# Kernel optimization log

Hardware: AMD Instinct MI355X
Metric: run time of the kernel (lower is better)

Reference implementation:

```python
import jax, jax.numpy as jnp
import numpy as np

N_NODES = 50000
N_EDGES = 800000
D_IN = 512
D_OUT = 128

def setup_inputs() -> dict:
    key = jax.random.key(0)
    k1, k2, k3, k4, k5, k6 = jax.random.split(key, 6)
    std = 1.0 / np.sqrt(D_OUT)
    x = jax.random.normal(k1, (N_NODES, D_IN), dtype=jnp.float32)
    edge_w = jax.random.uniform(k2, (N_EDGES,), dtype=jnp.float32)
    src = jax.random.randint(k3, (N_EDGES,), 0, N_NODES, dtype=jnp.int32)
    dst = jax.random.randint(k4, (N_EDGES,), 0, N_NODES, dtype=jnp.int32)
    W = jax.random.uniform(k5, (D_IN, D_OUT), minval=-std, maxval=std, dtype=jnp.float32)
    b = jax.random.uniform(k6, (D_OUT,), minval=-std, maxval=std, dtype=jnp.float32)
    return {"x": x, "edge_w": edge_w, "src": src, "dst": dst, "W": W, "b": b}

def reference(x, edge_w, src, dst, W, b):
    # Dense GEMM: [N, D_in] @ [D_in, D_out]
    h = x @ W
    # SpMM with COO adjacency: out[i] = sum_{e: dst[e]==i} edge_w[e] * h[src[e]]
    msg = h[src] * edge_w[:, None]          # [E, D_out]
    agg = jax.ops.segment_sum(msg, dst, num_segments=N_NODES)
    return agg + b
```

## Files before the change

### kernel.cpp

```cpp
#include <hip/hip_runtime.h>
#include <hip/hip_bf16.h>

#define M_NODES  50000
#define D_IN_K   512
#define D_OUT_N  128
#define N_EDGES  800000
#define SCAN_NBLK 49
#define PAD 16

typedef short  bf16x8 __attribute__((ext_vector_type(8)));
typedef float  f32x4  __attribute__((ext_vector_type(4)));

static __device__ __forceinline__ unsigned short f2bf(float f) {
    unsigned u = __float_as_uint(f);
    unsigned r = u + 0x7FFF + ((u >> 16) & 1);
    return (unsigned short)(r >> 16);
}
static __device__ __forceinline__ float bflo(unsigned q) { return __uint_as_float(q << 16); }
static __device__ __forceinline__ float bfhi(unsigned q) { return __uint_as_float(q & 0xFFFF0000u); }

__global__ __launch_bounds__(256) void permw_kernel(const float* __restrict__ W,
                                                    unsigned short* __restrict__ Wp) {
    int tid = blockIdx.x * 256 + threadIdx.x;
    int lane = tid & 63;
    int nt   = (tid >> 6) & 7;
    int kb4  = tid >> 9;
    int n    = nt * 16 + (lane & 15);
    int kbase = kb4 * 32 + ((lane >> 4) & 3) * 8;
    unsigned short frag[8];
#pragma unroll
    for (int j = 0; j < 8; ++j)
        frag[j] = f2bf(W[(size_t)(kbase + j) * D_OUT_N + n]);
    *(uint4*)&Wp[(size_t)tid * 8] = *(const uint4*)frag;
}

__global__ __launch_bounds__(256, 2) void mfma_gemm_hist_kernel(const float* __restrict__ x,
                                                                const uint4* __restrict__ Wp4,
                                                                unsigned short* __restrict__ h,
                                                                const int* __restrict__ dst,
                                                                int* __restrict__ counts) {
    __shared__ uint4 wlds[4096];

    const int wave = threadIdx.x >> 6;
    const int lane = threadIdx.x & 63;
    const int m0   = blockIdx.x * 128 + wave * 32;
    const int mrow = lane & 15;
    const int kgrp = lane >> 4;

    const int r0 = m0 + mrow;
    const int r1 = m0 + 16 + mrow;
    const float* xr0 = x + (size_t)((r0 < M_NODES) ? r0 : M_NODES - 1) * D_IN_K + kgrp * 8;
    const float* xr1 = x + (size_t)((r1 < M_NODES) ? r1 : M_NODES - 1) * D_IN_K + kgrp * 8;

    f32x4 acc[2][8];
#pragma unroll
    for (int f = 0; f < 2; ++f)
#pragma unroll
        for (int t = 0; t < 8; ++t) acc[f][t] = (f32x4){0.f, 0.f, 0.f, 0.f};

    for (int half = 0; half < 2; ++half) {
        __syncthreads();
#pragma unroll
        for (int i = 0; i < 16; ++i)
            wlds[threadIdx.x + i * 256] = Wp4[half * 4096 + threadIdx.x + i * 256];
        __syncthreads();

        const float* px0 = xr0 + half * 256;
        const float* px1 = xr1 + half * 256;

        float4 a00 = *(const float4*)(px0);
        float4 a01 = *(const float4*)(px0 + 4);
        float4 a10 = *(const float4*)(px1);
        float4 a11 = *(const float4*)(px1 + 4);

#pragma unroll
        for (int kb = 0; kb < 8; ++kb) {
            float4 n00, n01, n10, n11;
            if (kb < 7) {
                n00 = *(const float4*)(px0 + (kb + 1) * 32);
                n01 = *(const float4*)(px0 + (kb + 1) * 32 + 4);
                n10 = *(const float4*)(px1 + (kb + 1) * 32);
                n11 = *(const float4*)(px1 + (kb + 1) * 32 + 4);
            }

            union { bf16x8 v; __hip_bfloat162 h2[4]; } c0, c1;
            c0.h2[0] = __float22bfloat162_rn(make_float2(a00.x, a00.y));
            c0.h2[1] = __float22bfloat162_rn(make_float2(a00.z, a00.w));
            c0.h2[2] = __float22bfloat162_rn(make_float2(a01.x, a01.y));
            c0.h2[3] = __float22bfloat162_rn(make_float2(a01.z, a01.w));
            c1.h2[0] = __float22bfloat162_rn(make_float2(a10.x, a10.y));
            c1.h2[1] = __float22bfloat162_rn(make_float2(a10.z, a10.w));
            c1.h2[2] = __float22bfloat162_rn(make_float2(a11.x, a11.y));
            c1.h2[3] = __float22bfloat162_rn(make_float2(a11.z, a11.w));
            bf16x8 a0 = c0.v, a1 = c1.v;

#pragma unroll
            for (int nt = 0; nt < 8; ++nt) {
                union { uint4 u; bf16x8 v; } wb;
                wb.u = wlds[(kb * 8 + nt) * 64 + lane];
                acc[0][nt] = __builtin_amdgcn_mfma_f32_16x16x32_bf16(a0, wb.v, acc[0][nt], 0, 0, 0);
                acc[1][nt] = __builtin_amdgcn_mfma_f32_16x16x32_bf16(a1, wb.v, acc[1][nt], 0, 0, 0);
            }

            if (kb < 7) { a00 = n00; a01 = n01; a10 = n10; a11 = n11; }
        }
    }

#pragma unroll
    for (int f = 0; f < 2; ++f)
#pragma unroll
        for (int r = 0; r < 4; ++r) {
            int rr = m0 + f * 16 + kgrp * 4 + r;
            if (rr < M_NODES) {
                unsigned short* hp = h + (size_t)rr * D_OUT_N + mrow;
#pragma unroll
                for (int nt = 0; nt < 8; ++nt)
                    hp[nt * 16] = f2bf(acc[f][nt][r]);
            }
        }

    const int epb = (N_EDGES + gridDim.x - 1) / gridDim.x;
    const int e0  = blockIdx.x * epb;
    const int e1  = (e0 + epb < N_EDGES) ? e0 + epb : N_EDGES;
    for (int e = e0 + threadIdx.x; e < e1; e += 256)
        atomicAdd(&counts[dst[e] * PAD], 1);
}

__global__ __launch_bounds__(256) void scan_kernel(const int* __restrict__ counts,
                                                   int* __restrict__ offsets,
                                                   int* __restrict__ cursor,
                                                   int* __restrict__ partials,
                                                   int* __restrict__ flags) {
    __shared__ int wsum[4];
    __shared__ int carry_s;
    const int tid  = threadIdx.x;
    const int lane = tid & 63;
    const int wid  = tid >> 6;
    const int blk  = blockIdx.x;
    const int base = blk * 1024 + tid * 4;

    int v[4];
#pragma unroll
    for (int i = 0; i < 4; ++i)
        v[i] = (base + i < M_NODES) ? counts[(base + i) * PAD] : 0;
    int t = v[0] + v[1] + v[2] + v[3];

    int s = t;
#pragma unroll
    for (int d = 1; d < 64; d <<= 1) {
        int u = __shfl_up(s, d, 64);
        if (lane >= d) s += u;
    }
    if (lane == 63) wsum[wid] = s;
    __syncthreads();
    int wbase = 0;
#pragma unroll
    for (int w = 0; w < 4; ++w) wbase += (w < wid) ? wsum[w] : 0;
    int total = wsum[0] + wsum[1] + wsum[2] + wsum[3];

    if (tid == 0) {
        __hip_atomic_store(&partials[blk], total, __ATOMIC_RELAXED, __HIP_MEMORY_SCOPE_AGENT);
        __hip_atomic_store(&flags[blk], 1, __ATOMIC_RELEASE, __HIP_MEMORY_SCOPE_AGENT);
        if (blk == 0) offsets[M_NODES] = N_EDGES;
    }

    if (wid == 0) {
        int val = 0;
        if (lane < blk) {
            while (__hip_atomic_load(&flags[lane], __ATOMIC_ACQUIRE, __HIP_MEMORY_SCOPE_AGENT) == 0) {}
            val = __hip_atomic_load(&partials[lane], __ATOMIC_RELAXED, __HIP_MEMORY_SCOPE_AGENT);
        }
#pragma unroll
        for (int d = 32; d > 0; d >>= 1) val += __shfl_xor(val, d, 64);
        if (lane == 0) carry_s = val;
    }
    __syncthreads();
    const int carry = carry_s;

    int run = carry + wbase + s - t;
#pragma unroll
    for (int i = 0; i < 4; ++i) {
        if (base + i < M_NODES) {
            offsets[base + i] = run;
            cursor[(base + i) * PAD] = run;
        }
        run += v[i];
    }
}

__global__ __launch_bounds__(256) void fill_kernel(const int* __restrict__ src,
                                                   const int* __restrict__ dst,
                                                   const float* __restrict__ edge_w,
                                                   int* __restrict__ cursor,
                                                   int2* __restrict__ ep) {
    int e = blockIdx.x * blockDim.x + threadIdx.x;
    if (e >= N_EDGES) return;
    int d   = dst[e];
    int pos = atomicAdd(&cursor[d * PAD], 1);
    ep[pos] = make_int2(src[e], __float_as_int(edge_w[e]));
}

__global__ __launch_bounds__(256) void gather_kernel(const unsigned short* __restrict__ h,
                                                     const int2* __restrict__ ep,
                                                     const int* __restrict__ offsets,
                                                     const float* __restrict__ b,
                                                     float* __restrict__ out) {
    int t    = blockIdx.x * blockDim.x + threadIdx.x;
    int node = t >> 4;
    int lane = t & 15;
    if (node >= M_NODES) return;
    int beg = offsets[node];
    int end = offsets[node + 1];

    float4 b0 = *(const float4*)&b[lane * 8];
    float4 b1 = *(const float4*)&b[lane * 8 + 4];
    float a[4][8];
#pragma unroll
    for (int u = 0; u < 4; ++u)
#pragma unroll
        for (int c = 0; c < 8; ++c) a[u][c] = 0.f;

    int j = beg;
    for (; j + 4 <= end; j += 4) {
        int2 e0 = ep[j], e1 = ep[j + 1], e2 = ep[j + 2], e3 = ep[j + 3];
        uint4 q0 = *(const uint4*)(h + (size_t)e0.x * D_OUT_N + lane * 8);
        uint4 q1 = *(const uint4*)(h + (size_t)e1.x * D_OUT_N + lane * 8);
        uint4 q2 = *(const uint4*)(h + (size_t)e2.x * D_OUT_N + lane * 8);
        uint4 q3 = *(const uint4*)(h + (size_t)e3.x * D_OUT_N + lane * 8);
        float w0 = __int_as_float(e0.y), w1 = __int_as_float(e1.y);
        float w2 = __int_as_float(e2.y), w3 = __int_as_float(e3.y);
        a[0][0] += w0 * bflo(q0.x);  a[0][1] += w0 * bfhi(q0.x);
        a[0][2] += w0 * bflo(q0.y);  a[0][3] += w0 * bfhi(q0.y);
        a[0][4] += w0 * bflo(q0.z);  a[0][5] += w0 * bfhi(q0.z);
        a[0][6] += w0 * bflo(q0.w);  a[0][7] += w0 * bfhi(q0.w);
        a[1][0] += w1 * bflo(q1.x);  a[1][1] += w1 * bfhi(q1.x);
        a[1][2] += w1 * bflo(q1.y);  a[1][3] += w1 * bfhi(q1.y);
        a[1][4] += w1 * bflo(q1.z);  a[1][5] += w1 * bfhi(q1.z);
        a[1][6] += w1 * bflo(q1.w);  a[1][7] += w1 * bfhi(q1.w);
        a[2][0] += w2 * bflo(q2.x);  a[2][1] += w2 * bfhi(q2.x);
        a[2][2] += w2 * bflo(q2.y);  a[2][3] += w2 * bfhi(q2.y);
        a[2][4] += w2 * bflo(q2.z);  a[2][5] += w2 * bfhi(q2.z);
        a[2][6] += w2 * bflo(q2.w);  a[2][7] += w2 * bfhi(q2.w);
        a[3][0] += w3 * bflo(q3.x);  a[3][1] += w3 * bfhi(q3.x);
        a[3][2] += w3 * bflo(q3.y);  a[3][3] += w3 * bfhi(q3.y);
        a[3][4] += w3 * bflo(q3.z);  a[3][5] += w3 * bfhi(q3.z);
        a[3][6] += w3 * bflo(q3.w);  a[3][7] += w3 * bfhi(q3.w);
    }
    for (; j < end; ++j) {
        int2 e0 = ep[j];
        float w0 = __int_as_float(e0.y);
        uint4 q0 = *(const uint4*)(h + (size_t)e0.x * D_OUT_N + lane * 8);
        a[0][0] += w0 * bflo(q0.x);  a[0][1] += w0 * bfhi(q0.x);
        a[0][2] += w0 * bflo(q0.y);  a[0][3] += w0 * bfhi(q0.y);
        a[0][4] += w0 * bflo(q0.z);  a[0][5] += w0 * bfhi(q0.z);
        a[0][6] += w0 * bflo(q0.w);  a[0][7] += w0 * bfhi(q0.w);
    }

    float4 o0 = make_float4(b0.x + a[0][0] + a[1][0] + a[2][0] + a[3][0],
                            b0.y + a[0][1] + a[1][1] + a[2][1] + a[3][1],
                            b0.z + a[0][2] + a[1][2] + a[2][2] + a[3][2],
                            b0.w + a[0][3] + a[1][3] + a[2][3] + a[3][3]);
    float4 o1 = make_float4(b1.x + a[0][4] + a[1][4] + a[2][4] + a[3][4],
                            b1.y + a[0][5] + a[1][5] + a[2][5] + a[3][5],
                            b1.z + a[0][6] + a[1][6] + a[2][6] + a[3][6],
                            b1.w + a[0][7] + a[1][7] + a[2][7] + a[3][7]);
    float* op = &out[(size_t)node * D_OUT_N + lane * 8];
    *(float4*)op = o0;
    *(float4*)(op + 4) = o1;
}

extern "C" void kernel_launch(void* const* d_in, const int* in_sizes, int n_in,
                              void* d_out, int out_size, void* d_ws, size_t ws_size,
                              hipStream_t stream) {
    const float* x      = (const float*)d_in[0];
    const float* edge_w = (const float*)d_in[1];
    const int*   src    = (const int*)d_in[2];
    const int*   dst    = (const int*)d_in[3];
    const float* W      = (const float*)d_in[4];
    const float* b      = (const float*)d_in[5];
    float* out = (float*)d_out;

    char* wsp = (char*)d_ws;
    unsigned short* h = (unsigned short*)wsp;  wsp += (size_t)M_NODES * D_OUT_N * 2;
    int*   counts   = (int*)wsp;         wsp += (size_t)M_NODES * PAD * 4;
    int*   flags    = (int*)wsp;         wsp += 64 * 4;
    int*   cursor   = (int*)wsp;         wsp += (size_t)M_NODES * PAD * 4;
    int*   offsets  = (int*)wsp;         wsp += (((size_t)M_NODES + 1) * 4 + 15) & ~15ull;
    int2*  ep       = (int2*)wsp;        wsp += (size_t)N_EDGES * 8;
    unsigned short* Wp = (unsigned short*)wsp; wsp += (size_t)16 * 8 * 64 * 8 * 2;
    int*   partials = (int*)wsp;         wsp += (SCAN_NBLK * 4 + 15) & ~15ull;

    hipMemsetAsync(counts, 0, (size_t)M_NODES * PAD * 4 + 64 * 4, stream);
    permw_kernel<<<32, 256, 0, stream>>>(W, Wp);
    mfma_gemm_hist_kernel<<<(M_NODES + 127) / 128, 256, 0, stream>>>(
        x, (const uint4*)Wp, h, dst, counts);
    scan_kernel<<<SCAN_NBLK, 256, 0, stream>>>(counts, offsets, cursor, partials, flags);
    fill_kernel<<<(N_EDGES + 255) / 256, 256, 0, stream>>>(src, dst, edge_w, cursor, ep);
    gather_kernel<<<(int)(((long long)M_NODES * 16 + 255) / 256), 256, 0, stream>>>(
        h, ep, offsets, b, out);
}
```

Measured before the change: 290.4 us.

## Double-buffer W via direct global-to-LDS loads, shrink GEMM tiles, unpad counters

The GEMM kernel now streams W through a 2x16KB double buffer with global_load_lds, prefetching the next K chunk while computing the current one. It also halves the per-block M tile to 64 rows and raises the occupancy hint to 4 blocks per CU, so LDS per block shrinks and more blocks are resident. Separately, the per-node count and cursor arrays drop the 16-int padding, which shrinks the memset and lets the scan use vector loads, at the cost of more atomic contention on shared cache lines. Smaller tiles mean x-rows are reused across fewer N and more W traffic per row, and a barrier is added every chunk.

```diff
diff --git a/kernel.cpp b/kernel.cpp
--- a/kernel.cpp
+++ b/kernel.cpp
@@ -6,7 +6,6 @@
 #define D_OUT_N  128
 #define N_EDGES  800000
 #define SCAN_NBLK 49
-#define PAD 16
 
 typedef short  bf16x8 __attribute__((ext_vector_type(8)));
 typedef float  f32x4  __attribute__((ext_vector_type(4)));
@@ -18,6 +17,13 @@
 }
 static __device__ __forceinline__ float bflo(unsigned q) { return __uint_as_float(q << 16); }
 static __device__ __forceinline__ float bfhi(unsigned q) { return __uint_as_float(q & 0xFFFF0000u); }
+
+static __device__ __forceinline__ void gl2lds16(const uint4* g, uint4* l) {
+    __builtin_amdgcn_global_load_lds(
+        (const __attribute__((address_space(1))) void*)g,
+        (__attribute__((address_space(3))) void*)l,
+        16, 0, 0);
+}
 
 __global__ __launch_bounds__(256) void permw_kernel(const float* __restrict__ W,
                                                     unsigned short* __restrict__ Wp) {
@@ -34,96 +40,86 @@
     *(uint4*)&Wp[(size_t)tid * 8] = *(const uint4*)frag;
 }
 
-__global__ __launch_bounds__(256, 2) void mfma_gemm_hist_kernel(const float* __restrict__ x,
+__global__ __launch_bounds__(256, 4) void mfma_gemm_hist_kernel(const float* __restrict__ x,
                                                                 const uint4* __restrict__ Wp4,
                                                                 unsigned short* __restrict__ h,
                                                                 const int* __restrict__ dst,
                                                                 int* __restrict__ counts) {
-    __shared__ uint4 wlds[4096];
-
-    const int wave = threadIdx.x >> 6;
-    const int lane = threadIdx.x & 63;
-    const int m0   = blockIdx.x * 128 + wave * 32;
+    __shared__ uint4 wlds[2][1024];
+
+    const int tid  = threadIdx.x;
+    const int wave = tid >> 6;
+    const int lane = tid & 63;
+    const int m0   = blockIdx.x * 64 + wave * 16;
     const int mrow = lane & 15;
     const int kgrp = lane >> 4;
 
     const int r0 = m0 + mrow;
-    const int r1 = m0 + 16 + mrow;
     const float* xr0 = x + (size_t)((r0 < M_NODES) ? r0 : M_NODES - 1) * D_IN_K + kgrp * 8;
-    const float* xr1 = x + (size_t)((r1 < M_NODES) ? r1 : M_NODES - 1) * D_IN_K + kgrp * 8;
-
-    f32x4 acc[2][8];
-#pragma unroll
-    for (int f = 0; f < 2; ++f)
-#pragma unroll
-        for (int t = 0; t < 8; ++t) acc[f][t] = (f32x4){0.f, 0.f, 0.f, 0.f};
-
-    for (int half = 0; half < 2; ++half) {
-        __syncthreads();
-#pragma unroll
-        for (int i = 0; i < 16; ++i)
-            wlds[threadIdx.x + i * 256] = Wp4[half * 4096 + threadIdx.x + i * 256];
-        __syncthreads();
-
-        const float* px0 = xr0 + half * 256;
-        const float* px1 = xr1 + half * 256;
-
-        float4 a00 = *(const float4*)(px0);
-        float4 a01 = *(const float4*)(px0 + 4);
-        float4 a10 = *(const float4*)(px1);
-        float4 a11 = *(const float4*)(px1 + 4);
-
-#pragma unroll
-        for (int kb = 0; kb < 8; ++kb) {
-            float4 n00, n01, n10, n11;
-            if (kb < 7) {
-                n00 = *(const float4*)(px0 + (kb + 1) * 32);
-                n01 = *(const float4*)(px0 + (kb + 1) * 32 + 4);
-                n10 = *(const float4*)(px1 + (kb + 1) * 32);
-                n11 = *(const float4*)(px1 + (kb + 1) * 32 + 4);
+
+    f32x4 acc[8];
+#pragma unroll
+    for (int t = 0; t < 8; ++t) acc[t] = (f32x4){0.f, 0.f, 0.f, 0.f};
+
+#pragma unroll
+    for (int i = 0; i < 4; ++i)
+        gl2lds16(Wp4 + tid + i * 256, &wlds[0][tid + i * 256]);
+
+    float4 a0 = *(const float4*)(xr0);
+    float4 a1 = *(const float4*)(xr0 + 4);
+
+    __syncthreads();
+
+    for (int c = 0; c < 8; ++c) {
+        const int pb = c & 1;
+        if (c < 7) {
+#pragma unroll
+            for (int i = 0; i < 4; ++i)
+                gl2lds16(Wp4 + (c + 1) * 1024 + tid + i * 256,
+                         &wlds[pb ^ 1][tid + i * 256]);
+        }
+#pragma unroll
+        for (int kk = 0; kk < 2; ++kk) {
+            const int kb = c * 2 + kk;
+            float4 n0, n1;
+            if (kb < 15) {
+                const float* p = xr0 + (kb + 1) * 32;
+                n0 = *(const float4*)(p);
+                n1 = *(const float4*)(p + 4);
             }
-
-            union { bf16x8 v; __hip_bfloat162 h2[4]; } c0, c1;
-            c0.h2[0] = __float22bfloat162_rn(make_float2(a00.x, a00.y));
-            c0.h2[1] = __float22bfloat162_rn(make_float2(a00.z, a00.w));
-            c0.h2[2] = __float22bfloat162_rn(make_float2(a01.x, a01.y));
-            c0.h2[3] = __float22bfloat162_rn(make_float2(a01.z, a01.w));
-            c1.h2[0] = __float22bfloat162_rn(make_float2(a10.x, a10.y));
-            c1.h2[1] = __float22bfloat162_rn(make_float2(a10.z, a10.w));
-            c1.h2[2] = __float22bfloat162_rn(make_float2(a11.x, a11.y));
-            c1.h2[3] = __float22bfloat162_rn(make_float2(a11.z, a11.w));
-            bf16x8 a0 = c0.v, a1 = c1.v;
-
+            union { bf16x8 v; __hip_bfloat162 h2[4]; } cv;
+            cv.h2[0] = __float22bfloat162_rn(make_float2(a0.x, a0.y));
+            cv.h2[1] = __float22bfloat162_rn(make_float2(a0.z, a0.w));
+            cv.h2[2] = __float22bfloat162_rn(make_float2(a1.x, a1.y));
+            cv.h2[3] = __float22bfloat162_rn(make_float2(a1.z, a1.w));
+            bf16x8 af = cv.v;
 #pragma unroll
             for (int nt = 0; nt < 8; ++nt) {
                 union { uint4 u; bf16x8 v; } wb;
-                wb.u = wlds[(kb * 8 + nt) * 64 + lane];
-                acc[0][nt] = __builtin_amdgcn_mfma_f32_16x16x32_bf16(a0, wb.v, acc[0][nt], 0, 0, 0);
-                acc[1][nt] = __builtin_amdgcn_mfma_f32_16x16x32_bf16(a1, wb.v, acc[1][nt], 0, 0, 0);
+                wb.u = wlds[pb][kk * 512 + nt * 64 + lane];
+                acc[nt] = __builtin_amdgcn_mfma_f32_16x16x32_bf16(af, wb.v, acc[nt], 0, 0, 0);
             }
-
-            if (kb < 7) { a00 = n00; a01 = n01; a10 = n10; a11 = n11; }
-        }
-    }
-
-#pragma unroll
-    for (int f = 0; f < 2; ++f)
-#pragma unroll
-        for (int r = 0; r < 4; ++r) {
-            int rr = m0 + f * 16 + kgrp * 4 + r;
-            if (rr < M_NODES) {
-                unsigned short* hp = h + (size_t)rr * D_OUT_N + mrow;
-#pragma unroll
-                for (int nt = 0; nt < 8; ++nt)
-                    hp[nt * 16] = f2bf(acc[f][nt][r]);
-            }
-        }
+            if (kb < 15) { a0 = n0; a1 = n1; }
+        }
+        __syncthreads();
+    }
+
+#pragma unroll
+    for (int r = 0; r < 4; ++r) {
+        int rr = m0 + kgrp * 4 + r;
+        if (rr < M_NODES) {
+            unsigned short* hp = h + (size_t)rr * D_OUT_N + mrow;
+#pragma unroll
+            for (int nt = 0; nt < 8; ++nt)
+                hp[nt * 16] = f2bf(acc[nt][r]);
+        }
+    }
 
     const int epb = (N_EDGES + gridDim.x - 1) / gridDim.x;
     const int e0  = blockIdx.x * epb;
     const int e1  = (e0 + epb < N_EDGES) ? e0 + epb : N_EDGES;
-    for (int e = e0 + threadIdx.x; e < e1; e += 256)
-        atomicAdd(&counts[dst[e] * PAD], 1);
+    for (int e = e0 + tid; e < e1; e += 256)
+        atomicAdd(&counts[dst[e]], 1);
 }
 
 __global__ __launch_bounds__(256) void scan_kernel(const int* __restrict__ counts,
@@ -140,9 +136,14 @@
     const int base = blk * 1024 + tid * 4;
 
     int v[4];
-#pragma unroll
-    for (int i = 0; i < 4; ++i)
-        v[i] = (base + i < M_NODES) ? counts[(base + i) * PAD] : 0;
+    if (base + 3 < M_NODES) {
+        int4 q = *(const int4*)&counts[base];
+        v[0] = q.x; v[1] = q.y; v[2] = q.z; v[3] = q.w;
+    } else {
+#pragma unroll
+        for (int i = 0; i < 4; ++i)
+            v[i] = (base + i < M_NODES) ? counts[base + i] : 0;
+    }
     int t = v[0] + v[1] + v[2] + v[3];
 
     int s = t;
@@ -182,7 +183,7 @@
     for (int i = 0; i < 4; ++i) {
         if (base + i < M_NODES) {
             offsets[base + i] = run;
-            cursor[(base + i) * PAD] = run;
+            cursor[base + i]  = run;
         }
         run += v[i];
     }
@@ -196,7 +197,7 @@
     int e = blockIdx.x * blockDim.x + threadIdx.x;
     if (e >= N_EDGES) return;
     int d   = dst[e];
-    int pos = atomicAdd(&cursor[d * PAD], 1);
+    int pos = atomicAdd(&cursor[d], 1);
     ep[pos] = make_int2(src[e], __float_as_int(edge_w[e]));
 }
 
@@ -282,17 +283,17 @@
 
     char* wsp = (char*)d_ws;
     unsigned short* h = (unsigned short*)wsp;  wsp += (size_t)M_NODES * D_OUT_N * 2;
-    int*   counts   = (int*)wsp;         wsp += (size_t)M_NODES * PAD * 4;
+    int*   counts   = (int*)wsp;         wsp += (size_t)M_NODES * 4;
     int*   flags    = (int*)wsp;         wsp += 64 * 4;
-    int*   cursor   = (int*)wsp;         wsp += (size_t)M_NODES * PAD * 4;
+    int*   cursor   = (int*)wsp;         wsp += (size_t)M_NODES * 4;
     int*   offsets  = (int*)wsp;         wsp += (((size_t)M_NODES + 1) * 4 + 15) & ~15ull;
     int2*  ep       = (int2*)wsp;        wsp += (size_t)N_EDGES * 8;
     unsigned short* Wp = (unsigned short*)wsp; wsp += (size_t)16 * 8 * 64 * 8 * 2;
     int*   partials = (int*)wsp;         wsp += (SCAN_NBLK * 4 + 15) & ~15ull;
 
-    hipMemsetAsync(counts, 0, (size_t)M_NODES * PAD * 4 + 64 * 4, stream);
+    hipMemsetAsync(counts, 0, (size_t)M_NODES * 4 + 64 * 4, stream);
     permw_kernel<<<32, 256, 0, stream>>>(W, Wp);
-    mfma_gemm_hist_kernel<<<(M_NODES + 127) / 128, 256, 0, stream>>>(
+    mfma_gemm_hist_kernel<<<(M_NODES + 63) / 64, 256, 0, stream>>>(
         x, (const uint4*)Wp, h, dst, counts);
     scan_kernel<<<SCAN_NBLK, 256, 0, stream>>>(counts, offsets, cursor, partials, flags);
     fill_kernel<<<(N_EDGES + 255) / 256, 256, 0, stream>>>(src, dst, edge_w, cursor, ep);
```

After: 293.9 us. About the same (+1.2%).

## Replace padded per-node counters with 8 edge-range replicas for histogram and fill

Applied to the files above, without the earlier changes.

Replaces the 16-int padded per-node degree counters with 8 compact replicated count and cursor arrays, one for each 100k-edge segment. The scan kernel sums the replicas to get node degree and hands each replica its own starting cursor. The goal is to cut the memset size and the padded strided traffic, and to spread atomic contention across replicas. In exchange, neighbouring nodes now share cache lines in the compact arrays, and the scan reads eight times as many counters.

```diff
diff --git a/kernel.cpp b/kernel.cpp
--- a/kernel.cpp
+++ b/kernel.cpp
@@ -6,7 +6,8 @@
 #define D_OUT_N  128
 #define N_EDGES  800000
 #define SCAN_NBLK 49
-#define PAD 16
+#define NREP 8
+#define REP_SEG 100000
 
 typedef short  bf16x8 __attribute__((ext_vector_type(8)));
 typedef float  f32x4  __attribute__((ext_vector_type(4)));
@@ -38,7 +39,7 @@
                                                                 const uint4* __restrict__ Wp4,
                                                                 unsigned short* __restrict__ h,
                                                                 const int* __restrict__ dst,
-                                                                int* __restrict__ counts) {
+                                                                int* __restrict__ counts8) {
     __shared__ uint4 wlds[4096];
 
     const int wave = threadIdx.x >> 6;
@@ -122,13 +123,15 @@
     const int epb = (N_EDGES + gridDim.x - 1) / gridDim.x;
     const int e0  = blockIdx.x * epb;
     const int e1  = (e0 + epb < N_EDGES) ? e0 + epb : N_EDGES;
-    for (int e = e0 + threadIdx.x; e < e1; e += 256)
-        atomicAdd(&counts[dst[e] * PAD], 1);
-}
-
-__global__ __launch_bounds__(256) void scan_kernel(const int* __restrict__ counts,
+    for (int e = e0 + threadIdx.x; e < e1; e += 256) {
+        int rep = e / REP_SEG;
+        atomicAdd(&counts8[rep * M_NODES + dst[e]], 1);
+    }
+}
+
+__global__ __launch_bounds__(256) void scan_kernel(const int* __restrict__ counts8,
                                                    int* __restrict__ offsets,
-                                                   int* __restrict__ cursor,
+                                                   int* __restrict__ cursor8,
                                                    int* __restrict__ partials,
                                                    int* __restrict__ flags) {
     __shared__ int wsum[4];
@@ -139,11 +142,29 @@
     const int blk  = blockIdx.x;
     const int base = blk * 1024 + tid * 4;
 
-    int v[4];
-#pragma unroll
-    for (int i = 0; i < 4; ++i)
-        v[i] = (base + i < M_NODES) ? counts[(base + i) * PAD] : 0;
-    int t = v[0] + v[1] + v[2] + v[3];
+    int c[NREP][4];
+    if (base + 3 < M_NODES) {
+#pragma unroll
+        for (int x = 0; x < NREP; ++x) {
+            int4 q = *(const int4*)&counts8[x * M_NODES + base];
+            c[x][0] = q.x; c[x][1] = q.y; c[x][2] = q.z; c[x][3] = q.w;
+        }
+    } else {
+#pragma unroll
+        for (int x = 0; x < NREP; ++x)
+#pragma unroll
+            for (int i = 0; i < 4; ++i)
+                c[x][i] = (base + i < M_NODES) ? counts8[x * M_NODES + base + i] : 0;
+    }
+    int deg[4];
+#pragma unroll
+    for (int i = 0; i < 4; ++i) {
+        int d = 0;
+#pragma unroll
+        for (int x = 0; x < NREP; ++x) d += c[x][i];
+        deg[i] = d;
+    }
+    int t = deg[0] + deg[1] + deg[2] + deg[3];
 
     int s = t;
 #pragma unroll
@@ -182,21 +203,27 @@
     for (int i = 0; i < 4; ++i) {
         if (base + i < M_NODES) {
             offsets[base + i] = run;
-            cursor[(base + i) * PAD] = run;
-        }
-        run += v[i];
+            int acc = run;
+#pragma unroll
+            for (int x = 0; x < NREP; ++x) {
+                cursor8[x * M_NODES + base + i] = acc;
+                acc += c[x][i];
+            }
+        }
+        run += deg[i];
     }
 }
 
 __global__ __launch_bounds__(256) void fill_kernel(const int* __restrict__ src,
                                                    const int* __restrict__ dst,
                                                    const float* __restrict__ edge_w,
-                                                   int* __restrict__ cursor,
+                                                   int* __restrict__ cursor8,
                                                    int2* __restrict__ ep) {
     int e = blockIdx.x * blockDim.x + threadIdx.x;
     if (e >= N_EDGES) return;
+    int rep = e / REP_SEG;
     int d   = dst[e];
-    int pos = atomicAdd(&cursor[d * PAD], 1);
+    int pos = atomicAdd(&cursor8[rep * M_NODES + d], 1);
     ep[pos] = make_int2(src[e], __float_as_int(edge_w[e]));
 }
 
@@ -282,20 +309,20 @@
 
     char* wsp = (char*)d_ws;
     unsigned short* h = (unsigned short*)wsp;  wsp += (size_t)M_NODES * D_OUT_N * 2;
-    int*   counts   = (int*)wsp;         wsp += (size_t)M_NODES * PAD * 4;
+    int*   counts8  = (int*)wsp;         wsp += (size_t)NREP * M_NODES * 4;
     int*   flags    = (int*)wsp;         wsp += 64 * 4;
-    int*   cursor   = (int*)wsp;         wsp += (size_t)M_NODES * PAD * 4;
+    int*   cursor8  = (int*)wsp;         wsp += (size_t)NREP * M_NODES * 4;
     int*   offsets  = (int*)wsp;         wsp += (((size_t)M_NODES + 1) * 4 + 15) & ~15ull;
     int2*  ep       = (int2*)wsp;        wsp += (size_t)N_EDGES * 8;
     unsigned short* Wp = (unsigned short*)wsp; wsp += (size_t)16 * 8 * 64 * 8 * 2;
     int*   partials = (int*)wsp;         wsp += (SCAN_NBLK * 4 + 15) & ~15ull;
 
-    hipMemsetAsync(counts, 0, (size_t)M_NODES * PAD * 4 + 64 * 4, stream);
+    hipMemsetAsync(counts8, 0, (size_t)NREP * M_NODES * 4 + 64 * 4, stream);
     permw_kernel<<<32, 256, 0, stream>>>(W, Wp);
     mfma_gemm_hist_kernel<<<(M_NODES + 127) / 128, 256, 0, stream>>>(
-        x, (const uint4*)Wp, h, dst, counts);
-    scan_kernel<<<SCAN_NBLK, 256, 0, stream>>>(counts, offsets, cursor, partials, flags);
-    fill_kernel<<<(N_EDGES + 255) / 256, 256, 0, stream>>>(src, dst, edge_w, cursor, ep);
+        x, (const uint4*)Wp, h, dst, counts8);
+    scan_kernel<<<SCAN_NBLK, 256, 0, stream>>>(counts8, offsets, cursor8, partials, flags);
+    fill_kernel<<<(N_EDGES + 255) / 256, 256, 0, stream>>>(src, dst, edge_w, cursor8, ep);
     gather_kernel<<<(int)(((long long)M_NODES * 16 + 255) / 256), 256, 0, stream>>>(
         h, ep, offsets, b, out);
 }
```

New measurement: 291.2 us. No clear change (+0.3%).

## Replace per-node CSR sort with 128-node bucket sort and LDS scatter-add aggregation

Applied to the files above, without the earlier changes.

Replaces the per-node counting sort (per-node histogram, multi-block scan, per-edge global atomics) with a coarse bucket sort into 391 buckets of 128 destination nodes. Histograms are built in LDS, and the fill pass reserves space with one global atomic per bucket per block. Gather now runs one block per bucket and accumulates into a 64KB LDS tile with float atomics, then adds bias and writes rows contiguously. The aim is fewer global atomics and a much shorter scan, at the cost of LDS atomic contention, narrow 4-byte h loads per lane, and src packed into 16 bits, which truncates node indices above 65535.

```diff
diff --git a/kernel.cpp b/kernel.cpp
--- a/kernel.cpp
+++ b/kernel.cpp
@@ -5,8 +5,7 @@
 #define D_IN_K   512
 #define D_OUT_N  128
 #define N_EDGES  800000
-#define SCAN_NBLK 49
-#define PAD 16
+#define NBKT     391
 
 typedef short  bf16x8 __attribute__((ext_vector_type(8)));
 typedef float  f32x4  __attribute__((ext_vector_type(4)));
@@ -38,7 +37,7 @@
                                                                 const uint4* __restrict__ Wp4,
                                                                 unsigned short* __restrict__ h,
                                                                 const int* __restrict__ dst,
-                                                                int* __restrict__ counts) {
+                                                                int* __restrict__ bcounts) {
     __shared__ uint4 wlds[4096];
 
     const int wave = threadIdx.x >> 6;
@@ -119,33 +118,31 @@
             }
         }
 
+    __syncthreads();
+    int* lhist = (int*)wlds;
+    for (int k = threadIdx.x; k < NBKT; k += 256) lhist[k] = 0;
+    __syncthreads();
     const int epb = (N_EDGES + gridDim.x - 1) / gridDim.x;
     const int e0  = blockIdx.x * epb;
     const int e1  = (e0 + epb < N_EDGES) ? e0 + epb : N_EDGES;
     for (int e = e0 + threadIdx.x; e < e1; e += 256)
-        atomicAdd(&counts[dst[e] * PAD], 1);
-}
-
-__global__ __launch_bounds__(256) void scan_kernel(const int* __restrict__ counts,
-                                                   int* __restrict__ offsets,
-                                                   int* __restrict__ cursor,
-                                                   int* __restrict__ partials,
-                                                   int* __restrict__ flags) {
-    __shared__ int wsum[4];
-    __shared__ int carry_s;
+        atomicAdd(&lhist[dst[e] >> 7], 1);
+    __syncthreads();
+    for (int k = threadIdx.x; k < NBKT; k += 256) {
+        int c = lhist[k];
+        if (c) atomicAdd(&bcounts[k], c);
+    }
+}
+
+__global__ __launch_bounds__(512) void scan_bkt_kernel(const int* __restrict__ bcounts,
+                                                       int* __restrict__ boff,
+                                                       int* __restrict__ gcur) {
+    __shared__ int wsum[8];
     const int tid  = threadIdx.x;
     const int lane = tid & 63;
     const int wid  = tid >> 6;
-    const int blk  = blockIdx.x;
-    const int base = blk * 1024 + tid * 4;
-
-    int v[4];
-#pragma unroll
-    for (int i = 0; i < 4; ++i)
-        v[i] = (base + i < M_NODES) ? counts[(base + i) * PAD] : 0;
-    int t = v[0] + v[1] + v[2] + v[3];
-
-    int s = t;
+    int v = (tid < NBKT) ? bcounts[tid] : 0;
+    int s = v;
 #pragma unroll
     for (int d = 1; d < 64; d <<= 1) {
         int u = __shfl_up(s, d, 64);
@@ -153,120 +150,124 @@
     }
     if (lane == 63) wsum[wid] = s;
     __syncthreads();
-    int wbase = 0;
-#pragma unroll
-    for (int w = 0; w < 4; ++w) wbase += (w < wid) ? wsum[w] : 0;
-    int total = wsum[0] + wsum[1] + wsum[2] + wsum[3];
-
-    if (tid == 0) {
-        __hip_atomic_store(&partials[blk], total, __ATOMIC_RELAXED, __HIP_MEMORY_SCOPE_AGENT);
-        __hip_atomic_store(&flags[blk], 1, __ATOMIC_RELEASE, __HIP_MEMORY_SCOPE_AGENT);
-        if (blk == 0) offsets[M_NODES] = N_EDGES;
-    }
-
-    if (wid == 0) {
-        int val = 0;
-        if (lane < blk) {
-            while (__hip_atomic_load(&flags[lane], __ATOMIC_ACQUIRE, __HIP_MEMORY_SCOPE_AGENT) == 0) {}
-            val = __hip_atomic_load(&partials[lane], __ATOMIC_RELAXED, __HIP_MEMORY_SCOPE_AGENT);
-        }
-#pragma unroll
-        for (int d = 32; d > 0; d >>= 1) val += __shfl_xor(val, d, 64);
-        if (lane == 0) carry_s = val;
-    }
-    __syncthreads();
-    const int carry = carry_s;
-
-    int run = carry + wbase + s - t;
-#pragma unroll
-    for (int i = 0; i < 4; ++i) {
-        if (base + i < M_NODES) {
-            offsets[base + i] = run;
-            cursor[(base + i) * PAD] = run;
-        }
-        run += v[i];
-    }
-}
-
-__global__ __launch_bounds__(256) void fill_kernel(const int* __restrict__ src,
-                                                   const int* __restrict__ dst,
-                                                   const float* __restrict__ edge_w,
-                                                   int* __restrict__ cursor,
-                                                   int2* __restrict__ ep) {
-    int e = blockIdx.x * blockDim.x + threadIdx.x;
-    if (e >= N_EDGES) return;
-    int d   = dst[e];
-    int pos = atomicAdd(&cursor[d * PAD], 1);
-    ep[pos] = make_int2(src[e], __float_as_int(edge_w[e]));
-}
-
-__global__ __launch_bounds__(256) void gather_kernel(const unsigned short* __restrict__ h,
-                                                     const int2* __restrict__ ep,
-                                                     const int* __restrict__ offsets,
-                                                     const float* __restrict__ b,
-                                                     float* __restrict__ out) {
-    int t    = blockIdx.x * blockDim.x + threadIdx.x;
-    int node = t >> 4;
-    int lane = t & 15;
-    if (node >= M_NODES) return;
-    int beg = offsets[node];
-    int end = offsets[node + 1];
-
-    float4 b0 = *(const float4*)&b[lane * 8];
-    float4 b1 = *(const float4*)&b[lane * 8 + 4];
-    float a[4][8];
-#pragma unroll
-    for (int u = 0; u < 4; ++u)
-#pragma unroll
-        for (int c = 0; c < 8; ++c) a[u][c] = 0.f;
-
-    int j = beg;
-    for (; j + 4 <= end; j += 4) {
-        int2 e0 = ep[j], e1 = ep[j + 1], e2 = ep[j + 2], e3 = ep[j + 3];
-        uint4 q0 = *(const uint4*)(h + (size_t)e0.x * D_OUT_N + lane * 8);
-        uint4 q1 = *(const uint4*)(h + (size_t)e1.x * D_OUT_N + lane * 8);
-        uint4 q2 = *(const uint4*)(h + (size_t)e2.x * D_OUT_N + lane * 8);
-        uint4 q3 = *(const uint4*)(h + (size_t)e3.x * D_OUT_N + lane * 8);
+    int wb = 0;
+#pragma unroll
+    for (int w = 0; w < 8; ++w) wb += (w < wid) ? wsum[w] : 0;
+    int excl = wb + s - v;
+    if (tid < NBKT) { boff[tid] = excl; gcur[tid] = excl; }
+    if (tid == NBKT) boff[NBKT] = excl;
+}
+
+__global__ __launch_bounds__(256) void fill_bkt_kernel(const int* __restrict__ src,
+                                                       const int* __restrict__ dst,
+                                                       const float* __restrict__ edge_w,
+                                                       int* __restrict__ gcur,
+                                                       int2* __restrict__ eb) {
+    __shared__ int lh[NBKT];
+    __shared__ int lb[NBKT];
+    const int tid = threadIdx.x;
+    for (int k = tid; k < NBKT; k += 256) lh[k] = 0;
+    __syncthreads();
+
+    const int ebase = blockIdx.x * 2048 + tid * 8;
+    int d[8];
+#pragma unroll
+    for (int i = 0; i < 8; ++i) {
+        int e = ebase + i;
+        if (e < N_EDGES) {
+            d[i] = dst[e];
+            atomicAdd(&lh[d[i] >> 7], 1);
+        } else d[i] = -1;
+    }
+    __syncthreads();
+
+    for (int k = tid; k < NBKT; k += 256) {
+        int c = lh[k];
+        lb[k] = c ? atomicAdd(&gcur[k], c) : 0;
+        lh[k] = 0;
+    }
+    __syncthreads();
+
+#pragma unroll
+    for (int i = 0; i < 8; ++i) {
+        int e = ebase + i;
+        if (e < N_EDGES) {
+            int bk = d[i] >> 7;
+            int r  = atomicAdd(&lh[bk], 1);
+            eb[lb[bk] + r] = make_int2((src[e] & 0xFFFF) | ((d[i] & 127) << 16),
+                                       __float_as_int(edge_w[e]));
+        }
+    }
+}
+
+__global__ __launch_bounds__(256, 2) void gather_bkt_kernel(const unsigned short* __restrict__ h,
+                                                            const int2* __restrict__ eb,
+                                                            const int* __restrict__ boff,
+                                                            const float* __restrict__ b,
+                                                            float* __restrict__ out) {
+    __shared__ float lo[128 * 128];
+    const int tid  = threadIdx.x;
+    const int lane = tid & 63;
+    const int wave = tid >> 6;
+    const int k    = blockIdx.x;
+
+#pragma unroll
+    for (int i = 0; i < 16; ++i)
+        *(float4*)&lo[(tid + i * 256) * 4] = make_float4(0.f, 0.f, 0.f, 0.f);
+    __syncthreads();
+
+    const int ebeg = boff[k];
+    const int eend = boff[k + 1];
+    const int cnt  = eend - ebeg;
+    const int per  = (cnt + 3) >> 2;
+    int j    = ebeg + wave * per;
+    int jend = j + per; if (jend > eend) jend = eend;
+    const int c0 = lane * 2;
+
+    for (; j + 4 <= jend; j += 4) {
+        int2 e0 = eb[j], e1 = eb[j + 1], e2 = eb[j + 2], e3 = eb[j + 3];
+        unsigned q0 = *(const unsigned*)&h[(size_t)(e0.x & 0xFFFF) * D_OUT_N + c0];
+        unsigned q1 = *(const unsigned*)&h[(size_t)(e1.x & 0xFFFF) * D_OUT_N + c0];
+        unsigned q2 = *(const unsigned*)&h[(size_t)(e2.x & 0xFFFF) * D_OUT_N + c0];
+        unsigned q3 = *(const unsigned*)&h[(size_t)(e3.x & 0xFFFF) * D_OUT_N + c0];
         float w0 = __int_as_float(e0.y), w1 = __int_as_float(e1.y);
         float w2 = __int_as_float(e2.y), w3 = __int_as_float(e3.y);
-        a[0][0] += w0 * bflo(q0.x);  a[0][1] += w0 * bfhi(q0.x);
-        a[0][2] += w0 * bflo(q0.y);  a[0][3] += w0 * bfhi(q0.y);
-        a[0][4] += w0 * bflo(q0.z);  a[0][5] += w0 * bfhi(q0.z);
-        a[0][6] += w0 * bflo(q0.w);  a[0][7] += w0 * bfhi(q0.w);
-        a[1][0] += w1 * bflo(q1.x);  a[1][1] += w1 * bfhi(q1.x);
-        a[1][2] += w1 * bflo(q1.y);  a[1][3] += w1 * bfhi(q1.y);
-        a[1][4] += w1 * bflo(q1.z);  a[1][5] += w1 * bfhi(q1.z);
-        a[1][6] += w1 * bflo(q1.w);  a[1][7] += w1 * bfhi(q1.w);
-        a[2][0] += w2 * bflo(q2.x);  a[2][1] += w2 * bfhi(q2.x);
-        a[2][2] += w2 * bflo(q2.y);  a[2][3] += w2 * bfhi(q2.y);
-        a[2][4] += w2 * bflo(q2.z);  a[2][5] += w2 * bfhi(q2.z);
-        a[2][6] += w2 * bflo(q2.w);  a[2][7] += w2 * bfhi(q2.w);
-        a[3][0] += w3 * bflo(q3.x);  a[3][1] += w3 * bfhi(q3.x);
-        a[3][2] += w3 * bflo(q3.y);  a[3][3] += w3 * bfhi(q3.y);
-        a[3][4] += w3 * bflo(q3.z);  a[3][5] += w3 * bfhi(q3.z);
-        a[3][6] += w3 * bflo(q3.w);  a[3][7] += w3 * bfhi(q3.w);
-    }
-    for (; j < end; ++j) {
-        int2 e0 = ep[j];
+        int d0 = (e0.x >> 16) & 127, d1 = (e1.x >> 16) & 127;
+        int d2 = (e2.x >> 16) & 127, d3 = (e3.x >> 16) & 127;
+        atomicAdd(&lo[d0 * 128 + c0],     w0 * bflo(q0));
+        atomicAdd(&lo[d0 * 128 + c0 + 1], w0 * bfhi(q0));
+        atomicAdd(&lo[d1 * 128 + c0],     w1 * bflo(q1));
+        atomicAdd(&lo[d1 * 128 + c0 + 1], w1 * bfhi(q1));
+        atomicAdd(&lo[d2 * 128 + c0],     w2 * bflo(q2));
+        atomicAdd(&lo[d2 * 128 + c0 + 1], w2 * bfhi(q2));
+        atomicAdd(&lo[d3 * 128 + c0],     w3 * bflo(q3));
+        atomicAdd(&lo[d3 * 128 + c0 + 1], w3 * bfhi(q3));
+    }
+    for (; j < jend; ++j) {
+        int2 e0 = eb[j];
+        unsigned q0 = *(const unsigned*)&h[(size_t)(e0.x & 0xFFFF) * D_OUT_N + c0];
         float w0 = __int_as_float(e0.y);
-        uint4 q0 = *(const uint4*)(h + (size_t)e0.x * D_OUT_N + lane * 8);
-        a[0][0] += w0 * bflo(q0.x);  a[0][1] += w0 * bfhi(q0.x);
-        a[0][2] += w0 * bflo(q0.y);  a[0][3] += w0 * bfhi(q0.y);
-        a[0][4] += w0 * bflo(q0.z);  a[0][5] += w0 * bfhi(q0.z);
-        a[0][6] += w0 * bflo(q0.w);  a[0][7] += w0 * bfhi(q0.w);
-    }
-
-    float4 o0 = make_float4(b0.x + a[0][0] + a[1][0] + a[2][0] + a[3][0],
-                            b0.y + a[0][1] + a[1][1] + a[2][1] + a[3][1],
-                            b0.z + a[0][2] + a[1][2] + a[2][2] + a[3][2],
-                            b0.w + a[0][3] + a[1][3] + a[2][3] + a[3][3]);
-    float4 o1 = make_float4(b1.x + a[0][4] + a[1][4] + a[2][4] + a[3][4],
-                            b1.y + a[0][5] + a[1][5] + a[2][5] + a[3][5],
-                            b1.z + a[0][6] + a[1][6] + a[2][6] + a[3][6],
-                            b1.w + a[0][7] + a[1][7] + a[2][7] + a[3][7]);
-    float* op = &out[(size_t)node * D_OUT_N + lane * 8];
-    *(float4*)op = o0;
-    *(float4*)(op + 4) = o1;
+        int d0 = (e0.x >> 16) & 127;
+        atomicAdd(&lo[d0 * 128 + c0],     w0 * bflo(q0));
+        atomicAdd(&lo[d0 * 128 + c0 + 1], w0 * bfhi(q0));
+    }
+    __syncthreads();
+
+    const int nl   = tid >> 1;
+    const int hf   = tid & 1;
+    const int node = k * 128 + nl;
+    if (node < M_NODES) {
+        const float*  ls = &lo[nl * 128 + hf * 64];
+        const float4* bp = (const float4*)(b + hf * 64);
+        float*        op = &out[(size_t)node * D_OUT_N + hf * 64];
+#pragma unroll
+        for (int i = 0; i < 16; ++i) {
+            float4 v = ((const float4*)ls)[i];
+            float4 bb = bp[i];
+            v.x += bb.x; v.y += bb.y; v.z += bb.z; v.w += bb.w;
+            ((float4*)op)[i] = v;
+        }
+    }
 }
 
 extern "C" void kernel_launch(void* const* d_in, const int* in_sizes, int n_in,
@@ -282,20 +283,17 @@
 
     char* wsp = (char*)d_ws;
     unsigned short* h = (unsigned short*)wsp;  wsp += (size_t)M_NODES * D_OUT_N * 2;
-    int*   counts   = (int*)wsp;         wsp += (size_t)M_NODES * PAD * 4;
-    int*   flags    = (int*)wsp;         wsp += 64 * 4;
-    int*   cursor   = (int*)wsp;         wsp += (size_t)M_NODES * PAD * 4;
-    int*   offsets  = (int*)wsp;         wsp += (((size_t)M_NODES + 1) * 4 + 15) & ~15ull;
-    int2*  ep       = (int2*)wsp;        wsp += (size_t)N_EDGES * 8;
+    int2*  eb       = (int2*)wsp;        wsp += (size_t)N_EDGES * 8;
     unsigned short* Wp = (unsigned short*)wsp; wsp += (size_t)16 * 8 * 64 * 8 * 2;
-    int*   partials = (int*)wsp;         wsp += (SCAN_NBLK * 4 + 15) & ~15ull;
-
-    hipMemsetAsync(counts, 0, (size_t)M_NODES * PAD * 4 + 64 * 4, stream);
+    int*   bcounts  = (int*)wsp;         wsp += (NBKT * 4 + 15) & ~15;
+    int*   boff     = (int*)wsp;         wsp += ((NBKT + 1) * 4 + 15) & ~15;
+    int*   gcur     = (int*)wsp;         wsp += (NBKT * 4 + 15) & ~15;
+
+    hipMemsetAsync(bcounts, 0, NBKT * 4, stream);
     permw_kernel<<<32, 256, 0, stream>>>(W, Wp);
     mfma_gemm_hist_kernel<<<(M_NODES + 127) / 128, 256, 0, stream>>>(
-        x, (const uint4*)Wp, h, dst, counts);
-    scan_kernel<<<SCAN_NBLK, 256, 0, stream>>>(counts, offsets, cursor, partials, flags);
-    fill_kernel<<<(N_EDGES + 255) / 256, 256, 0, stream>>>(src, dst, edge_w, cursor, ep);
-    gather_kernel<<<(int)(((long long)M_NODES * 16 + 255) / 256), 256, 0, stream>>>(
-        h, ep, offsets, b, out);
-}
+        x, (const uint4*)Wp, h, dst, bcounts);
+    scan_bkt_kernel<<<1, 512, 0, stream>>>(bcounts, boff, gcur);
+    fill_bkt_kernel<<<(N_EDGES + 2047) / 2048, 256, 0, stream>>>(src, dst, edge_w, gcur, eb);
+    gather_bkt_kernel<<<NBKT, 256, 0, stream>>>(h, eb, boff, b, out);
+}
```

New measurement: 898.2 us. 3.09x slower.
